# Kernel tuning notes

Measured on AMD Instinct MI355X. Metric: run time of the kernel, lower is better.

## Reference

```python
import jax, jax.numpy as jnp
import numpy as np

N_NODES = 100000
D_FEAT = 128
N_ETYPES = 3
N_EDGES = 1000000


def setup_inputs() -> dict:
    key = jax.random.key(0)
    kx, ke = jax.random.split(key)
    x = jax.random.normal(kx, (N_NODES, D_FEAT), dtype=jnp.float32)
    # edges[t, 0] = src node ids, edges[t, 1] = dst node ids for edge type t
    edges = jax.random.randint(ke, (N_ETYPES, 2, N_EDGES), 0, N_NODES, dtype=jnp.int32)
    return {"x": x, "edges": edges}


def _copy_u_mean(x, src, dst, n_nodes):
    # gather source features and segment-mean them onto destination nodes;
    # nodes with zero in-degree get 0 (matching DGL copy_u + mean semantics)
    summed = jax.ops.segment_sum(x[src], dst, num_segments=n_nodes)  # [N, D]
    count = jax.ops.segment_sum(jnp.ones_like(dst, dtype=x.dtype), dst,
                                num_segments=n_nodes)  # [N]
    return jnp.where(count[:, None] > 0, summed / jnp.maximum(count, 1)[:, None],
                     jnp.zeros((), dtype=x.dtype))


def reference(x, edges):
    # sep=True: prepend the raw features before the per-edge-type aggregations
    parts = [x]
    for t in range(N_ETYPES):  # small fixed loop over structurally distinct edge types
        parts.append(_copy_u_mean(x, edges[t, 0], edges[t, 1], x.shape[0]))
    return jnp.concatenate(parts, axis=-1)  # [N, D*(1+N_ETYPES)]
```

## Files before the change

kernel.cpp:

```cpp
#include <hip/hip_runtime.h>
#include <hip/hip_bf16.h>

#define NN 100000
#define DF 128
#define NT 3
#define NE 1000000
#define DOUT 512
#define TOTH (NT * NN)
#define NBKT2 293
#define BCAP2 11264
#define CHUNK4 1024
#define CPT 245
#define CVT_BLOCKS (NN * DF / 2 / 256)
#define EDGE4_BLOCKS ((NT * NE / 4 + 255) / 256)
#define SCAN_CHUNK 1024
#define NB1 ((TOTH + SCAN_CHUNK - 1) / SCAN_CHUNK)
#define NXCD 8
#define SLICE_BINS (TOTH / NXCD)

typedef __attribute__((ext_vector_type(4))) float f4v;
typedef __attribute__((ext_vector_type(2))) float f2v;
__device__ __forceinline__ void nts_f4(float4 v, float4* p) {
    f4v t; t.x = v.x; t.y = v.y; t.z = v.z; t.w = v.w;
    __builtin_nontemporal_store(t, (f4v*)p);
}
__device__ __forceinline__ void nts_f2(float2 v, float2* p) {
    f2v t; t.x = v.x; t.y = v.y;
    __builtin_nontemporal_store(t, (f2v*)p);
}

__global__ __launch_bounds__(256) void zero_k(int* __restrict__ p, int n) {
    int i = blockIdx.x * 256 + threadIdx.x;
    if (i < n) p[i] = 0;
}

__global__ __launch_bounds__(256) void cvt_copy_k(const float2* __restrict__ x2,
                                                  unsigned int* __restrict__ xh,
                                                  float2* __restrict__ out2) {
    int i = blockIdx.x * 256 + threadIdx.x;
    float2 v = x2[i];
    __hip_bfloat162 h = __float22bfloat162_rn(v);
    xh[i] = *(unsigned int*)&h;
    int n = i >> 6;
    nts_f2(v, &out2[(size_t)n * (DOUT / 2) + (i & 63)]);
}

__global__ __launch_bounds__(256) void part_k(const int4* __restrict__ edges4,
                                              int* __restrict__ gcur,
                                              int2* __restrict__ append) {
    __shared__ int cntB[512];
    __shared__ int startB[512];
    __shared__ int curB[512];
    __shared__ int targB[512];
    __shared__ int s[256];
    __shared__ int2 staged[4096];
    const int n4row = NE / 4;
    int t = blockIdx.x / CPT;
    int c = blockIdx.x - t * CPT;
    int base4 = c * CHUNK4;
    int n4 = n4row - base4; if (n4 > CHUNK4) n4 = CHUNK4;
    int tid = threadIdx.x;
    for (int i = tid; i < 512; i += 256) { cntB[i] = 0; curB[i] = 0; }
    __syncthreads();

    int4 sv[4], dv[4];
    bool have[4];
#pragma unroll
    for (int j = 0; j < 4; j++) {
        int i4 = tid + j * 256;
        have[j] = (i4 < n4);
        if (have[j]) {
            sv[j] = edges4[(size_t)(2 * t) * n4row + base4 + i4];
            dv[j] = edges4[(size_t)(2 * t + 1) * n4row + base4 + i4];
            int b0 = t * NN;
            atomicAdd(&cntB[(b0 + dv[j].x) >> 10], 1);
            atomicAdd(&cntB[(b0 + dv[j].y) >> 10], 1);
            atomicAdd(&cntB[(b0 + dv[j].z) >> 10], 1);
            atomicAdd(&cntB[(b0 + dv[j].w) >> 10], 1);
        }
    }
    __syncthreads();
    int e0 = cntB[2 * tid], e1 = cntB[2 * tid + 1];
    int sum2 = e0 + e1;
    s[tid] = sum2;
    __syncthreads();
    for (int off = 1; off < 256; off <<= 1) {
        int tt = (tid >= off) ? s[tid - off] : 0;
        __syncthreads();
        s[tid] += tt;
        __syncthreads();
    }
    int run = s[tid] - sum2;
    startB[2 * tid] = run;
    startB[2 * tid + 1] = run + e0;
    __syncthreads();
#pragma unroll
    for (int j = 0; j < 4; j++) {
        if (have[j]) {
            int b0 = t * NN;
            int bin, b, p;
            bin = b0 + dv[j].x; b = bin >> 10; p = startB[b] + atomicAdd(&curB[b], 1); staged[p] = make_int2(sv[j].x, bin);
            bin = b0 + dv[j].y; b = bin >> 10; p = startB[b] + atomicAdd(&curB[b], 1); staged[p] = make_int2(sv[j].y, bin);
            bin = b0 + dv[j].z; b = bin >> 10; p = startB[b] + atomicAdd(&curB[b], 1); staged[p] = make_int2(sv[j].z, bin);
            bin = b0 + dv[j].w; b = bin >> 10; p = startB[b] + atomicAdd(&curB[b], 1); staged[p] = make_int2(sv[j].w, bin);
        }
    }
    __syncthreads();
    for (int i = tid; i < NBKT2; i += 256)
        if (cntB[i] > 0) targB[i] = atomicAdd(&gcur[i], cntB[i]);
    __syncthreads();
    int total = n4 * 4;
    for (int i = tid; i < total; i += 256) {
        int2 e = staged[i];
        int b = e.y >> 10;
        int gpos = targB[b] + (i - startB[b]);
        if (gpos < BCAP2) append[(size_t)b * BCAP2 + gpos] = e;
    }
}

__global__ __launch_bounds__(512) void scanB_k(const int* __restrict__ gcur,
                                               int* __restrict__ bucketStart) {
    __shared__ int s[512];
    int tid = threadIdx.x;
    int v = 0;
    if (tid < NBKT2) { v = gcur[tid]; if (v > BCAP2) v = BCAP2; }
    s[tid] = v;
    __syncthreads();
    for (int off = 1; off < 512; off <<= 1) {
        int tt = (tid >= off) ? s[tid - off] : 0;
        __syncthreads();
        s[tid] += tt;
        __syncthreads();
    }
    if (tid < NBKT2) bucketStart[tid] = s[tid] - v;
}

__global__ __launch_bounds__(256) void binz_k(const int* __restrict__ gcur,
                                              const int* __restrict__ bucketStart,
                                              const int2* __restrict__ append,
                                              int* __restrict__ srcS,
                                              int* __restrict__ cnt,
                                              int* __restrict__ offs) {
    __shared__ int lcnt[1024], lofs[1024], lcur[1024];
    __shared__ int s[256];
    int bkt = blockIdx.x;
    int tid = threadIdx.x;
    int nb = gcur[bkt]; if (nb > BCAP2) nb = BCAP2;
    for (int i = tid; i < 1024; i += 256) { lcnt[i] = 0; lcur[i] = 0; }
    __syncthreads();
    const int2* ap = append + (size_t)bkt * BCAP2;
    for (int i = tid; i < nb; i += 256) atomicAdd(&lcnt[ap[i].y & 1023], 1);
    __syncthreads();
    int b4 = tid * 4;
    int v0 = lcnt[b4], v1 = lcnt[b4 + 1], v2 = lcnt[b4 + 2], v3 = lcnt[b4 + 3];
    int sum = v0 + v1 + v2 + v3;
    s[tid] = sum;
    __syncthreads();
    for (int off = 1; off < 256; off <<= 1) {
        int tt = (tid >= off) ? s[tid - off] : 0;
        __syncthreads();
        s[tid] += tt;
        __syncthreads();
    }
    int run = s[tid] - sum;
    lofs[b4] = run; run += v0;
    lofs[b4 + 1] = run; run += v1;
    lofs[b4 + 2] = run; run += v2;
    lofs[b4 + 3] = run;
    __syncthreads();
    int gbase = bucketStart[bkt];
    int binBase = bkt << 10;
    for (int i = tid; i < 1024 && binBase + i < TOTH; i += 256) {
        cnt[binBase + i] = lcnt[i];
        offs[binBase + i] = gbase + lofs[i];
    }
    for (int i = tid; i < nb; i += 256) {
        int2 e = ap[i];
        int lb = e.y & 1023;
        int pos = lofs[lb] + atomicAdd(&lcur[lb], 1);
        srcS[gbase + pos] = e.x;
    }
}

__global__ __launch_bounds__(256) void gather_agg_k(const uint2* __restrict__ xh2,
                                                    const int* __restrict__ cnt,
                                                    const int* __restrict__ offs,
                                                    const int* __restrict__ srcS,
                                                    float4* __restrict__ out4) {
    int gtid = blockIdx.x * 256 + threadIdx.x;
    int a = gtid >> 6;
    if (a >= TOTH) return;
    int lane = threadIdx.x & 63;
    int half = lane >> 5;
    int col = lane & 31;
    int t = a / NN;
    int n = a - t * NN;
    int c = cnt[a];
    int base = offs[a];
    float4 acc = make_float4(0.f, 0.f, 0.f, 0.f);
    int k = half;
    for (; k + 6 < c; k += 8) {
        int s0 = srcS[base + k];
        int s1 = srcS[base + k + 2];
        int s2 = srcS[base + k + 4];
        int s3 = srcS[base + k + 6];
        uint2 u0 = xh2[(size_t)s0 * 32 + col];
        uint2 u1 = xh2[(size_t)s1 * 32 + col];
        uint2 u2 = xh2[(size_t)s2 * 32 + col];
        uint2 u3 = xh2[(size_t)s3 * 32 + col];
        float2 p;
        p = __bfloat1622float2(*(__hip_bfloat162*)&u0.x); acc.x += p.x; acc.y += p.y;
        p = __bfloat1622float2(*(__hip_bfloat162*)&u0.y); acc.z += p.x; acc.w += p.y;
        p = __bfloat1622float2(*(__hip_bfloat162*)&u1.x); acc.x += p.x; acc.y += p.y;
        p = __bfloat1622float2(*(__hip_bfloat162*)&u1.y); acc.z += p.x; acc.w += p.y;
        p = __bfloat1622float2(*(__hip_bfloat162*)&u2.x); acc.x += p.x; acc.y += p.y;
        p = __bfloat1622float2(*(__hip_bfloat162*)&u2.y); acc.z += p.x; acc.w += p.y;
        p = __bfloat1622float2(*(__hip_bfloat162*)&u3.x); acc.x += p.x; acc.y += p.y;
        p = __bfloat1622float2(*(__hip_bfloat162*)&u3.y); acc.z += p.x; acc.w += p.y;
    }
    for (; k < c; k += 2) {
        int s0 = srcS[base + k];
        uint2 u0 = xh2[(size_t)s0 * 32 + col];
        float2 p;
        p = __bfloat1622float2(*(__hip_bfloat162*)&u0.x); acc.x += p.x; acc.y += p.y;
        p = __bfloat1622float2(*(__hip_bfloat162*)&u0.y); acc.z += p.x; acc.w += p.y;
    }
    acc.x += __shfl_xor(acc.x, 32, 64);
    acc.y += __shfl_xor(acc.y, 32, 64);
    acc.z += __shfl_xor(acc.z, 32, 64);
    acc.w += __shfl_xor(acc.w, 32, 64);
    if (half == 0) {
        float sc = (c > 0) ? 1.0f / (float)c : 0.0f;
        acc.x *= sc; acc.y *= sc; acc.z *= sc; acc.w *= sc;
        nts_f4(acc, &out4[(size_t)n * (DOUT / 4) + (DF / 4) + t * (DF / 4) + col]);
    }
}


__global__ __launch_bounds__(256) void hist_k(const int4* __restrict__ edges4,
                                              int* __restrict__ hist) {
    int i = blockIdx.x * 256 + threadIdx.x;
    if (i >= NT * NE / 4) return;
    int t = i / (NE / 4);
    int e4 = i - t * (NE / 4);
    int4 d = edges4[(size_t)(2 * t + 1) * (NE / 4) + e4];
    atomicAdd(&hist[t * NN + d.x], 1);
    atomicAdd(&hist[t * NN + d.y], 1);
    atomicAdd(&hist[t * NN + d.z], 1);
    atomicAdd(&hist[t * NN + d.w], 1);
}

__global__ __launch_bounds__(256) void scan1_k(const int* __restrict__ hist,
                                               int* __restrict__ offs,
                                               int* __restrict__ bsum) {
    __shared__ int s[256];
    int tid = threadIdx.x;
    int base = blockIdx.x * SCAN_CHUNK + tid * 4;
    int v0 = 0, v1 = 0, v2 = 0, v3 = 0;
    if (base + 0 < TOTH) v0 = hist[base + 0];
    if (base + 1 < TOTH) v1 = hist[base + 1];
    if (base + 2 < TOTH) v2 = hist[base + 2];
    if (base + 3 < TOTH) v3 = hist[base + 3];
    int sum = v0 + v1 + v2 + v3;
    s[tid] = sum;
    __syncthreads();
    for (int off = 1; off < 256; off <<= 1) {
        int t = (tid >= off) ? s[tid - off] : 0;
        __syncthreads();
        s[tid] += t;
        __syncthreads();
    }
    int run = s[tid] - sum;
    if (tid == 255) bsum[blockIdx.x] = s[255];
    if (base + 0 < TOTH) { offs[base + 0] = run; run += v0; }
    if (base + 1 < TOTH) { offs[base + 1] = run; run += v1; }
    if (base + 2 < TOTH) { offs[base + 2] = run; run += v2; }
    if (base + 3 < TOTH) { offs[base + 3] = run; run += v3; }
}

__global__ __launch_bounds__(512) void scan2_k(int* __restrict__ bsum) {
    __shared__ int s[512];
    int tid = threadIdx.x;
    int v = (tid < NB1) ? bsum[tid] : 0;
    s[tid] = v;
    __syncthreads();
    for (int off = 1; off < 512; off <<= 1) {
        int t = (tid >= off) ? s[tid - off] : 0;
        __syncthreads();
        s[tid] += t;
        __syncthreads();
    }
    if (tid < NB1) bsum[tid] = s[tid] - v;
}

__global__ __launch_bounds__(256) void scan3_k(int* __restrict__ offs,
                                               const int* __restrict__ bsum) {
    int i = blockIdx.x * 256 + threadIdx.x;
    if (i < TOTH) offs[i] += bsum[i / SCAN_CHUNK];
}

__global__ __launch_bounds__(256) void fill_csr_k(const int4* __restrict__ edges4,
                                                  int* __restrict__ offs,
                                                  int* __restrict__ srcS) {
    int slice = blockIdx.x & (NXCD - 1);
    int i = (blockIdx.x >> 3) * 256 + threadIdx.x;
    if (i >= NT * NE / 4) return;
    int t = i / (NE / 4);
    int e4 = i - t * (NE / 4);
    int4 sv = edges4[(size_t)(2 * t) * (NE / 4) + e4];
    int4 dv = edges4[(size_t)(2 * t + 1) * (NE / 4) + e4];
    int b0 = t * NN;
    int bin;
    bin = b0 + dv.x; if (bin / SLICE_BINS == slice) srcS[atomicAdd(&offs[bin], 1)] = sv.x;
    bin = b0 + dv.y; if (bin / SLICE_BINS == slice) srcS[atomicAdd(&offs[bin], 1)] = sv.y;
    bin = b0 + dv.z; if (bin / SLICE_BINS == slice) srcS[atomicAdd(&offs[bin], 1)] = sv.z;
    bin = b0 + dv.w; if (bin / SLICE_BINS == slice) srcS[atomicAdd(&offs[bin], 1)] = sv.w;
}

__global__ __launch_bounds__(256) void gather_f32_k(const float4* __restrict__ x4,
                                                    const int* __restrict__ cnt,
                                                    const int* __restrict__ offs,
                                                    const int* __restrict__ srcS,
                                                    float4* __restrict__ out4) {
    int gtid = blockIdx.x * 256 + threadIdx.x;
    int w = gtid >> 6;
    int lane = threadIdx.x & 63;
    int half = lane >> 5;
    int col = lane & 31;
    if (w < NN / 2) {
        int n = 2 * w + half;
        out4[(size_t)n * (DOUT / 4) + col] = x4[(size_t)n * (DF / 4) + col];
        return;
    }
    int a = w - NN / 2;
    if (a >= TOTH) return;
    int t = a / NN;
    int n = a - t * NN;
    int c = cnt[a];
    int base = offs[a] - c;
    float4 acc = make_float4(0.f, 0.f, 0.f, 0.f);
    for (int k = half; k < c; k += 2) {
        int s0 = srcS[base + k];
        float4 v0 = x4[(size_t)s0 * (DF / 4) + col];
        acc.x += v0.x; acc.y += v0.y; acc.z += v0.z; acc.w += v0.w;
    }
    acc.x += __shfl_xor(acc.x, 32, 64);
    acc.y += __shfl_xor(acc.y, 32, 64);
    acc.z += __shfl_xor(acc.z, 32, 64);
    acc.w += __shfl_xor(acc.w, 32, 64);
    if (half == 0) {
        float sc = (c > 0) ? 1.0f / (float)c : 0.0f;
        acc.x *= sc; acc.y *= sc; acc.z *= sc; acc.w *= sc;
        out4[(size_t)n * (DOUT / 4) + (DF / 4) + t * (DF / 4) + col] = acc;
    }
}

extern "C" void kernel_launch(void* const* d_in, const int* in_sizes, int n_in,
                              void* d_out, int out_size, void* d_ws, size_t ws_size,
                              hipStream_t stream) {
    const float* x = (const float*)d_in[0];
    const int* edges = (const int*)d_in[1];
    float4* out4 = (float4*)d_out;

    const int covBlocks = (TOTH + 255) / 256;
    const int aggBlocks = (TOTH * 64 + 255) / 256;

    size_t appendInts = (size_t)NBKT2 * BCAP2 * 2;
    size_t fastInts = 1024 + appendInts + 2 * (size_t)TOTH +
                      (size_t)NN * DF / 2 + (size_t)NT * NE + 64;
    if (ws_size >= fastInts * 4) {
        int* gcur = (int*)d_ws;
        int* bucketStart = gcur + 512;
        int2* append = (int2*)(bucketStart + 512);
        int* cnt = (int*)d_ws + 1024 + appendInts;
        int* offs = cnt + TOTH;
        unsigned int* xh = (unsigned int*)(offs + TOTH);
        int* srcS = (int*)(xh + (size_t)NN * DF / 2);

        hipLaunchKernelGGL(zero_k, dim3(2), dim3(256), 0, stream, gcur, 512);
        hipLaunchKernelGGL(cvt_copy_k, dim3(CVT_BLOCKS), dim3(256), 0, stream,
                           (const float2*)x, xh, (float2*)d_out);
        hipLaunchKernelGGL(part_k, dim3(NT * CPT), dim3(256), 0, stream,
                           (const int4*)edges, gcur, append);
        hipLaunchKernelGGL(scanB_k, dim3(1), dim3(512), 0, stream, gcur, bucketStart);
        hipLaunchKernelGGL(binz_k, dim3(NBKT2), dim3(256), 0, stream,
                           gcur, bucketStart, append, srcS, cnt, offs);
        hipLaunchKernelGGL(gather_agg_k, dim3(aggBlocks), dim3(256), 0, stream,
                           (const uint2*)xh, cnt, offs, srcS, out4);
        return;
    }

    int* hist = (int*)d_ws;
    int* offs = hist + TOTH;
    int* bsum = offs + TOTH;
    int* srcS = bsum + 1024;
    const int nWaves = NN / 2 + TOTH;
    const int gatherBlocks = (nWaves + 3) / 4;
    hipLaunchKernelGGL(zero_k, dim3(covBlocks), dim3(256), 0, stream, hist, TOTH);
    hipLaunchKernelGGL(hist_k, dim3(EDGE4_BLOCKS), dim3(256), 0, stream,
                       (const int4*)edges, hist);
    hipLaunchKernelGGL(scan1_k, dim3(NB1), dim3(256), 0, stream, hist, offs, bsum);
    hipLaunchKernelGGL(scan2_k, dim3(1), dim3(512), 0, stream, bsum);
    hipLaunchKernelGGL(scan3_k, dim3(covBlocks), dim3(256), 0, stream, offs, bsum);
    hipLaunchKernelGGL(fill_csr_k, dim3(EDGE4_BLOCKS * NXCD), dim3(256), 0, stream,
                       (const int4*)edges, offs, srcS);
    hipLaunchKernelGGL(gather_f32_k, dim3(gatherBlocks), dim3(256), 0, stream,
                       (const float4*)x, hist, offs, srcS, out4);
}
```

Measured before the change: 222.6 us.

## Fuse bf16 conversion into partition kernel and pack per-bin count/offset

Merges the x-to-bf16 conversion and output copy into the edge partition launch, so the first blocks do the conversion and the remaining blocks partition edges. This removes one launch and lets the two independent phases overlap. The conversion is widened to float4 loads and stores, and per-bin count and offset are packed into one int2 array so the gather kernel does a single load. The conversion blocks now carry the large shared-memory allocation of the partition path, which may reduce their occupancy.

After: 218.6 us. Within noise of the previous version (-1.8%).

```diff
diff --git a/kernel.cpp b/kernel.cpp
--- a/kernel.cpp
+++ b/kernel.cpp
@@ -11,7 +11,7 @@
 #define BCAP2 11264
 #define CHUNK4 1024
 #define CPT 245
-#define CVT_BLOCKS (NN * DF / 2 / 256)
+#define CVT4_BLOCKS (NN * DF / 4 / 256)
 #define EDGE4_BLOCKS ((NT * NE / 4 + 255) / 256)
 #define SCAN_CHUNK 1024
 #define NB1 ((TOTH + SCAN_CHUNK - 1) / SCAN_CHUNK)
@@ -19,44 +19,45 @@
 #define SLICE_BINS (TOTH / NXCD)
 
 typedef __attribute__((ext_vector_type(4))) float f4v;
-typedef __attribute__((ext_vector_type(2))) float f2v;
 __device__ __forceinline__ void nts_f4(float4 v, float4* p) {
     f4v t; t.x = v.x; t.y = v.y; t.z = v.z; t.w = v.w;
     __builtin_nontemporal_store(t, (f4v*)p);
 }
-__device__ __forceinline__ void nts_f2(float2 v, float2* p) {
-    f2v t; t.x = v.x; t.y = v.y;
-    __builtin_nontemporal_store(t, (f2v*)p);
-}
 
 __global__ __launch_bounds__(256) void zero_k(int* __restrict__ p, int n) {
     int i = blockIdx.x * 256 + threadIdx.x;
     if (i < n) p[i] = 0;
 }
 
-__global__ __launch_bounds__(256) void cvt_copy_k(const float2* __restrict__ x2,
-                                                  unsigned int* __restrict__ xh,
-                                                  float2* __restrict__ out2) {
-    int i = blockIdx.x * 256 + threadIdx.x;
-    float2 v = x2[i];
-    __hip_bfloat162 h = __float22bfloat162_rn(v);
-    xh[i] = *(unsigned int*)&h;
-    int n = i >> 6;
-    nts_f2(v, &out2[(size_t)n * (DOUT / 2) + (i & 63)]);
-}
-
-__global__ __launch_bounds__(256) void part_k(const int4* __restrict__ edges4,
-                                              int* __restrict__ gcur,
-                                              int2* __restrict__ append) {
+__global__ __launch_bounds__(256) void cvtpart_k(const float4* __restrict__ x4,
+                                                 uint2* __restrict__ xh2,
+                                                 float4* __restrict__ out4,
+                                                 const int4* __restrict__ edges4,
+                                                 int* __restrict__ gcur,
+                                                 int2* __restrict__ append) {
     __shared__ int cntB[512];
     __shared__ int startB[512];
     __shared__ int curB[512];
     __shared__ int targB[512];
     __shared__ int s[256];
     __shared__ int2 staged[4096];
+
+    if (blockIdx.x < CVT4_BLOCKS) {
+        int i = blockIdx.x * 256 + threadIdx.x;
+        float4 v = x4[i];
+        __hip_bfloat162 h0 = __float22bfloat162_rn(make_float2(v.x, v.y));
+        __hip_bfloat162 h1 = __float22bfloat162_rn(make_float2(v.z, v.w));
+        uint2 u; u.x = *(unsigned int*)&h0; u.y = *(unsigned int*)&h1;
+        xh2[i] = u;
+        int n = i >> 5;
+        nts_f4(v, &out4[(size_t)n * (DOUT / 4) + (i & 31)]);
+        return;
+    }
+
     const int n4row = NE / 4;
-    int t = blockIdx.x / CPT;
-    int c = blockIdx.x - t * CPT;
+    int b = blockIdx.x - CVT4_BLOCKS;
+    int t = b / CPT;
+    int c = b - t * CPT;
     int base4 = c * CHUNK4;
     int n4 = n4row - base4; if (n4 > CHUNK4) n4 = CHUNK4;
     int tid = threadIdx.x;
@@ -98,11 +99,11 @@
     for (int j = 0; j < 4; j++) {
         if (have[j]) {
             int b0 = t * NN;
-            int bin, b, p;
-            bin = b0 + dv[j].x; b = bin >> 10; p = startB[b] + atomicAdd(&curB[b], 1); staged[p] = make_int2(sv[j].x, bin);
-            bin = b0 + dv[j].y; b = bin >> 10; p = startB[b] + atomicAdd(&curB[b], 1); staged[p] = make_int2(sv[j].y, bin);
-            bin = b0 + dv[j].z; b = bin >> 10; p = startB[b] + atomicAdd(&curB[b], 1); staged[p] = make_int2(sv[j].z, bin);
-            bin = b0 + dv[j].w; b = bin >> 10; p = startB[b] + atomicAdd(&curB[b], 1); staged[p] = make_int2(sv[j].w, bin);
+            int bin, bb, p;
+            bin = b0 + dv[j].x; bb = bin >> 10; p = startB[bb] + atomicAdd(&curB[bb], 1); staged[p] = make_int2(sv[j].x, bin);
+            bin = b0 + dv[j].y; bb = bin >> 10; p = startB[bb] + atomicAdd(&curB[bb], 1); staged[p] = make_int2(sv[j].y, bin);
+            bin = b0 + dv[j].z; bb = bin >> 10; p = startB[bb] + atomicAdd(&curB[bb], 1); staged[p] = make_int2(sv[j].z, bin);
+            bin = b0 + dv[j].w; bb = bin >> 10; p = startB[bb] + atomicAdd(&curB[bb], 1); staged[p] = make_int2(sv[j].w, bin);
         }
     }
     __syncthreads();
@@ -112,9 +113,9 @@
     int total = n4 * 4;
     for (int i = tid; i < total; i += 256) {
         int2 e = staged[i];
-        int b = e.y >> 10;
-        int gpos = targB[b] + (i - startB[b]);
-        if (gpos < BCAP2) append[(size_t)b * BCAP2 + gpos] = e;
+        int bb = e.y >> 10;
+        int gpos = targB[bb] + (i - startB[bb]);
+        if (gpos < BCAP2) append[(size_t)bb * BCAP2 + gpos] = e;
     }
 }
 
@@ -139,8 +140,7 @@
                                               const int* __restrict__ bucketStart,
                                               const int2* __restrict__ append,
                                               int* __restrict__ srcS,
-                                              int* __restrict__ cnt,
-                                              int* __restrict__ offs) {
+                                              int2* __restrict__ cntoffs) {
     __shared__ int lcnt[1024], lofs[1024], lcur[1024];
     __shared__ int s[256];
     int bkt = blockIdx.x;
@@ -170,10 +170,8 @@
     __syncthreads();
     int gbase = bucketStart[bkt];
     int binBase = bkt << 10;
-    for (int i = tid; i < 1024 && binBase + i < TOTH; i += 256) {
-        cnt[binBase + i] = lcnt[i];
-        offs[binBase + i] = gbase + lofs[i];
-    }
+    for (int i = tid; i < 1024 && binBase + i < TOTH; i += 256)
+        cntoffs[binBase + i] = make_int2(lcnt[i], gbase + lofs[i]);
     for (int i = tid; i < nb; i += 256) {
         int2 e = ap[i];
         int lb = e.y & 1023;
@@ -183,8 +181,7 @@
 }
 
 __global__ __launch_bounds__(256) void gather_agg_k(const uint2* __restrict__ xh2,
-                                                    const int* __restrict__ cnt,
-                                                    const int* __restrict__ offs,
+                                                    const int2* __restrict__ cntoffs,
                                                     const int* __restrict__ srcS,
                                                     float4* __restrict__ out4) {
     int gtid = blockIdx.x * 256 + threadIdx.x;
@@ -195,8 +192,9 @@
     int col = lane & 31;
     int t = a / NN;
     int n = a - t * NN;
-    int c = cnt[a];
-    int base = offs[a];
+    int2 co = cntoffs[a];
+    int c = co.x;
+    int base = co.y;
     float4 acc = make_float4(0.f, 0.f, 0.f, 0.f);
     int k = half;
     for (; k + 6 < c; k += 8) {
@@ -372,21 +370,19 @@
         int* gcur = (int*)d_ws;
         int* bucketStart = gcur + 512;
         int2* append = (int2*)(bucketStart + 512);
-        int* cnt = (int*)d_ws + 1024 + appendInts;
-        int* offs = cnt + TOTH;
-        unsigned int* xh = (unsigned int*)(offs + TOTH);
+        int2* cntoffs = (int2*)((int*)d_ws + 1024 + appendInts);
+        unsigned int* xh = (unsigned int*)(cntoffs + TOTH);
         int* srcS = (int*)(xh + (size_t)NN * DF / 2);
 
         hipLaunchKernelGGL(zero_k, dim3(2), dim3(256), 0, stream, gcur, 512);
-        hipLaunchKernelGGL(cvt_copy_k, dim3(CVT_BLOCKS), dim3(256), 0, stream,
-                           (const float2*)x, xh, (float2*)d_out);
-        hipLaunchKernelGGL(part_k, dim3(NT * CPT), dim3(256), 0, stream,
+        hipLaunchKernelGGL(cvtpart_k, dim3(CVT4_BLOCKS + NT * CPT), dim3(256), 0,
+                           stream, (const float4*)x, (uint2*)xh, (float4*)d_out,
                            (const int4*)edges, gcur, append);
         hipLaunchKernelGGL(scanB_k, dim3(1), dim3(512), 0, stream, gcur, bucketStart);
         hipLaunchKernelGGL(binz_k, dim3(NBKT2), dim3(256), 0, stream,
-                           gcur, bucketStart, append, srcS, cnt, offs);
+                           gcur, bucketStart, append, srcS, cntoffs);
         hipLaunchKernelGGL(gather_agg_k, dim3(aggBlocks), dim3(256), 0, stream,
-                           (const uint2*)xh, cnt, offs, srcS, out4);
+                           (const uint2*)xh, cntoffs, srcS, out4);
         return;
     }
 
```
